# Performance work log

Measured on AMD Instinct MI355X. Metric: run time of the kernel, lower is better.

## Reference

```python
import jax, jax.numpy as jnp
import numpy as np

HEADS, DH, HID, EDGE_D = 8, 16, 128, 32  # heads, head_dim, hidden_dim, edge_dim
N, E = 50000, 800000


def _ln(x, w, b):
    mu = jnp.mean(x, axis=-1, keepdims=True)
    var = jnp.var(x, axis=-1, keepdims=True)
    return (x - mu) * jax.lax.rsqrt(var + 1e-5) * w + b


def setup_inputs() -> dict:
    key = jax.random.key(0)
    ks = jax.random.split(key, 16)
    lin = lambda k, fi, fo: (jax.random.normal(k, (fi, fo), jnp.float32) / np.sqrt(fi).astype(np.float32))
    inp = {
        'x': jax.random.normal(ks[0], (N, HID), jnp.float32),
        'edge_index': jax.random.randint(ks[1], (2, E), 0, N, jnp.int32),
        'edge_attr': jax.random.normal(ks[2], (E, EDGE_D), jnp.float32),
        'Wq': lin(ks[3], HID, HID), 'bq': jnp.zeros((HID,), jnp.float32),
        'Wk': lin(ks[4], HID, HID), 'bk': jnp.zeros((HID,), jnp.float32),
        'Wv': lin(ks[5], HID, HID), 'bv': jnp.zeros((HID,), jnp.float32),
        'We': lin(ks[6], EDGE_D, HID), 'be': jnp.zeros((HID,), jnp.float32),
        'Wskip': lin(ks[7], HID, HID), 'bskip': jnp.zeros((HID,), jnp.float32),
        'ln1_w': jnp.ones((HID,), jnp.float32), 'ln1_b': jnp.zeros((HID,), jnp.float32),
        'W1': lin(ks[8], HID, 4 * HID), 'b1': jnp.zeros((4 * HID,), jnp.float32),
        'W2': lin(ks[9], 4 * HID, HID), 'b2': jnp.zeros((HID,), jnp.float32),
        'ln2_w': jnp.ones((HID,), jnp.float32), 'ln2_b': jnp.zeros((HID,), jnp.float32),
    }
    return inp


def reference(x, edge_index, edge_attr, Wq, bq, Wk, bk, Wv, bv, We, be,
              Wskip, bskip, ln1_w, ln1_b, W1, b1, W2, b2, ln2_w, ln2_b):
    n = x.shape[0]
    src, dst = edge_index[0], edge_index[1]

    h = _ln(x, ln1_w, ln1_b)
    # projections, then per-edge gathers -> [E, H, Dh]
    q = (h @ Wq + bq)[dst].reshape(-1, HEADS, DH)
    k = (h @ Wk + bk)[src].reshape(-1, HEADS, DH)
    v = (h @ Wv + bv)[src].reshape(-1, HEADS, DH)
    e = (edge_attr @ We + be).reshape(-1, HEADS, DH)
    k = k + e
    v = v + e

    alpha = jnp.einsum('ehd,ehd->eh', q, k) / np.sqrt(DH).astype(np.float32)  # [E, H]
    # segment softmax over destination nodes (PyG softmax semantics)
    amax = jax.ops.segment_max(alpha, dst, num_segments=n)
    amax = jnp.where(jnp.isfinite(amax), amax, 0.0)
    expa = jnp.exp(alpha - amax[dst])
    denom = jax.ops.segment_sum(expa, dst, num_segments=n)
    alpha = expa / (denom[dst] + 1e-16)

    msg = jax.ops.segment_sum(alpha[..., None] * v, dst, num_segments=n)  # [N, H, Dh]
    conv_out = msg.reshape(n, HID) + h @ Wskip + bskip  # root_weight skip

    x = x + conv_out
    h2 = _ln(x, ln2_w, ln2_b)
    ffn = jax.nn.gelu(h2 @ W1 + b1, approximate=False) @ W2 + b2
    return x + ffn
```

## Files before the change

kernel.cpp:

```cpp
#include <hip/hip_runtime.h>
#include <math.h>

#define HID 128
#define EDGE_D 32
#define SC 0.36067376f

typedef unsigned short u16;
typedef unsigned int u32;
typedef __bf16 bf16x8 __attribute__((ext_vector_type(8)));
typedef float f32x4 __attribute__((ext_vector_type(4)));
typedef u32 u32x4 __attribute__((ext_vector_type(4)));
typedef u32 u32x2 __attribute__((ext_vector_type(2)));

static __device__ __forceinline__ u16 f2bf(float f) {
  u32 u = __float_as_uint(f);
  u += 0x7fffu + ((u >> 16) & 1u);
  return (u16)(u >> 16);
}
static __device__ __forceinline__ u32 pack2(float a, float b) {
  return (u32)f2bf(a) | ((u32)f2bf(b) << 16);
}
static __device__ __forceinline__ float bflo(u32 w) { return __uint_as_float(w << 16); }
static __device__ __forceinline__ float bfhi(u32 w) { return __uint_as_float(w & 0xffff0000u); }
static __device__ __forceinline__ float grp16_sum(float x) {
  x += __int_as_float(__builtin_amdgcn_mov_dpp(__float_as_int(x), 0x128, 0xf, 0xf, true));
  x += __int_as_float(__builtin_amdgcn_mov_dpp(__float_as_int(x), 0x124, 0xf, 0xf, true));
  x += __int_as_float(__builtin_amdgcn_mov_dpp(__float_as_int(x), 0x122, 0xf, 0xf, true));
  x += __int_as_float(__builtin_amdgcn_mov_dpp(__float_as_int(x), 0x121, 0xf, 0xf, true));
  return x;
}
static __device__ __forceinline__ float wave_allreduce_sum(float v) {
#pragma unroll
  for (int off = 32; off > 0; off >>= 1) v += __shfl_xor(v, off);
  return v;
}

__global__ __launch_bounds__(256) void ln_kernel(const float* __restrict__ in,
                                                 u16* __restrict__ out,
                                                 const float* __restrict__ w,
                                                 const float* __restrict__ b, int n) {
  int row0 = blockIdx.x * 4 + (threadIdx.x >> 6);
  int lane = threadIdx.x & 63;
  int stride = gridDim.x * 4;
  for (int row = row0; row < n; row += stride) {
    const float* p = in + (size_t)row * HID;
    float a = p[lane], c = p[lane + 64];
    float s = wave_allreduce_sum(a + c);
    float s2 = wave_allreduce_sum(a * a + c * c);
    float mean = s * (1.f / 128.f);
    float var = s2 * (1.f / 128.f) - mean * mean;
    float rs = rsqrtf(var + 1e-5f);
    u16* o = out + (size_t)row * HID;
    o[lane] = f2bf((a - mean) * rs * w[lane] + b[lane]);
    o[lane + 64] = f2bf((c - mean) * rs * w[lane + 64] + b[lane + 64]);
  }
}

__global__ __launch_bounds__(256) void convert_weights(
    const float* __restrict__ Wq, const float* __restrict__ Wk,
    const float* __restrict__ Wv, const float* __restrict__ Ws,
    const float* __restrict__ W1, const float* __restrict__ W2,
    const float* __restrict__ We, u16* __restrict__ WqkvsT,
    u16* __restrict__ W1T, u16* __restrict__ W2T, u16* __restrict__ WbdT,
    int* __restrict__ cnt, int Nn) {
  int idx = blockIdx.x * 256 + threadIdx.x;
  if (idx < 65536) {
    int m = idx >> 7, k = idx & 127;
    const float* Wm = m < 128 ? Wq : m < 256 ? Wk : m < 384 ? Wv : Ws;
    WqkvsT[idx] = f2bf(Wm[k * 128 + (m & 127)]);
  } else if (idx < 131072) {
    int j = idx - 65536;
    int m = j >> 7, k = j & 127;
    W1T[j] = f2bf(W1[k * 512 + m]);
  } else if (idx < 196608) {
    int j = idx - 131072;
    int m = j >> 9, k = j & 511;
    W2T[j] = f2bf(W2[k * 128 + m]);
  } else if (idx < 229376) {
    int j = idx - 196608;
    int m = j >> 8, c = j & 255;
    WbdT[j] = ((c >> 5) == (m >> 4)) ? f2bf(We[(c & 31) * 128 + m]) : (u16)0;
  } else if (idx < 229376 + Nn) {
    cnt[idx - 229376] = 0;
  }
}

#define GSTAGE(buf, kc)                                                        \
  {                                                                            \
    _Pragma("unroll") for (int i = 0; i < 2; i++) {                            \
      int idx = i * 256 + t;                                                   \
      int row = idx >> 2, c4 = idx & 3;                                        \
      __builtin_amdgcn_global_load_lds(                                        \
          (const __attribute__((address_space(1))) u32*)(A + (size_t)(r0 + row) * K + (kc) + c4 * 8), \
          (__attribute__((address_space(3))) u32*)&As[buf][idx * 8], 16, 0, 0);\
      __builtin_amdgcn_global_load_lds(                                        \
          (const __attribute__((address_space(1))) u32*)(Bt + (size_t)(c0 + row) * K + (kc) + c4 * 8), \
          (__attribute__((address_space(3))) u32*)&Bs[buf][idx * 8], 16, 0, 0);\
    }                                                                          \
  }

#define GEMM_CORE                                                              \
  constexpr int NT = K / 32;                                                   \
  GSTAGE(0, 0)                                                                 \
  __syncthreads();                                                             \
  _Pragma("unroll") for (int tt = 0; tt < NT; tt++) {                          \
    if (tt + 1 < NT) GSTAGE((tt + 1) & 1, (tt + 1) * 32)                       \
    bf16x8 a0 = *(const bf16x8*)&As[tt & 1][(w * 32 + sr) * 32 + g * 8];       \
    bf16x8 a1 = *(const bf16x8*)&As[tt & 1][(w * 32 + 16 + sr) * 32 + g * 8];  \
    _Pragma("unroll") for (int nn = 0; nn < 8; nn++) {                         \
      bf16x8 b = *(const bf16x8*)&Bs[tt & 1][(nn * 16 + sr) * 32 + g * 8];     \
      acc[0][nn] = __builtin_amdgcn_mfma_f32_16x16x32_bf16(a0, b, acc[0][nn], 0, 0, 0); \
      acc[1][nn] = __builtin_amdgcn_mfma_f32_16x16x32_bf16(a1, b, acc[1][nn], 0, 0, 0); \
    }                                                                          \
    __syncthreads();                                                           \
  }

template <int EPI, int K>
__global__ __launch_bounds__(256) void gemm_bf16(
    const u16* __restrict__ A, const u16* __restrict__ Bt, int n,
    const float* __restrict__ bias0, const float* __restrict__ bias1,
    const float* __restrict__ bias2, const float* __restrict__ bias3,
    float* __restrict__ of0, u32* __restrict__ opq, u32* __restrict__ pkv,
    u16* __restrict__ ob1, const float* __restrict__ addsrc) {
  __shared__ u16 As[2][128 * 32];
  __shared__ u16 Bs[2][128 * 32];
  int t = threadIdx.x;
  int w = t >> 6, lane = t & 63;
  int g = lane >> 4, sr = lane & 15;
  int r0 = blockIdx.x * 128;
  int c0 = blockIdx.y * 128;
  f32x4 acc[2][8];
#pragma unroll
  for (int m = 0; m < 2; m++)
#pragma unroll
    for (int nn = 0; nn < 8; nn++) acc[m][nn] = {0.f, 0.f, 0.f, 0.f};

  GEMM_CORE

  if (EPI == 0 && blockIdx.y == 0) {
#pragma unroll
    for (int m = 0; m < 2; m++)
#pragma unroll
      for (int nn = 0; nn < 4; nn++)
#pragma unroll
        for (int j = 0; j < 4; j++) {
          int row = r0 + w * 32 + m * 16 + g * 4 + j;
          if (row < n) {
            int cj = nn * 16 + sr;
            opq[((size_t)row << 6) + cj] =
                pack2(acc[m][nn][j] + bias0[cj], acc[m][nn + 4][j] + bias0[cj + 64]);
          }
        }
    return;
  }
  if (EPI == 0 && (blockIdx.y == 1 || blockIdx.y == 2)) {
    const float* bp = blockIdx.y == 1 ? bias1 : bias2;
    int which = blockIdx.y - 1;
#pragma unroll
    for (int m = 0; m < 2; m++)
#pragma unroll
      for (int nn = 0; nn < 4; nn++)
#pragma unroll
        for (int j = 0; j < 4; j++) {
          int row = r0 + w * 32 + m * 16 + g * 4 + j;
          if (row < n) {
            int cj = nn * 16 + sr;
            pkv[((size_t)row << 7) + (cj << 1) + which] =
                pack2(acc[m][nn][j] + bp[cj], acc[m][nn + 4][j] + bp[cj + 64]);
          }
        }
    return;
  }
#pragma unroll
  for (int m = 0; m < 2; m++)
#pragma unroll
    for (int nn = 0; nn < 8; nn++)
#pragma unroll
      for (int j = 0; j < 4; j++) {
        int row = r0 + w * 32 + m * 16 + g * 4 + j;
        if (row < n) {
          int cj = nn * 16 + sr;
          float val = acc[m][nn][j];
          if (EPI == 0) {
            of0[(size_t)row * HID + cj] = val + bias3[cj];
          } else if (EPI == 1) {
            int cjg = blockIdx.y * 128 + cj;
            float v2 = val + bias0[cjg];
            v2 = 0.5f * v2 * (1.f + erff(v2 * 0.70710678118f));
            ob1[(size_t)row * 512 + cjg] = f2bf(v2);
          } else {
            of0[(size_t)row * HID + cj] = val + bias0[cj] + addsrc[(size_t)row * HID + cj];
          }
        }
      }
}

__global__ __launch_bounds__(256) void gemm_bd_fin(
    const u16* __restrict__ A, const u16* __restrict__ Bt, int n,
    const float* __restrict__ x, const float* __restrict__ msg,
    const float* __restrict__ lbuf, const float* __restrict__ be,
    const float* __restrict__ lnw, const float* __restrict__ lnb,
    float* __restrict__ skipx1, u16* __restrict__ h2) {
  __shared__ u16 As[2][128 * 32];
  __shared__ u16 Bs[2][128 * 32];
  constexpr int K = 256;
  int t = threadIdx.x;
  int w = t >> 6, lane = t & 63;
  int g = lane >> 4, sr = lane & 15;
  int r0 = blockIdx.x * 128;
  int c0 = 0;
  f32x4 acc[2][8];
#pragma unroll
  for (int m = 0; m < 2; m++)
#pragma unroll
    for (int nn = 0; nn < 8; nn++) acc[m][nn] = {0.f, 0.f, 0.f, 0.f};

  GEMM_CORE

  float becol[8], wcol[8], bcol[8];
#pragma unroll
  for (int nn = 0; nn < 8; nn++) {
    int c = nn * 16 + sr;
    becol[nn] = be[c];
    wcol[nn] = lnw[c];
    bcol[nn] = lnb[c];
  }
#pragma unroll
  for (int m = 0; m < 2; m++)
#pragma unroll
    for (int j = 0; j < 4; j++) {
      int row = r0 + w * 32 + m * 16 + g * 4 + j;
      if (row < n) {
        const float* xr = x + (size_t)row * HID;
        const float* mr = msg + (size_t)row * HID;
        float* sxr = skipx1 + (size_t)row * HID;
        f32x4 L0 = *(const f32x4*)(lbuf + (size_t)row * 8);
        f32x4 L1 = *(const f32x4*)(lbuf + (size_t)row * 8 + 4);
        float tv[8];
        float s = 0.f, s2 = 0.f;
#pragma unroll
        for (int nn = 0; nn < 8; nn++) {
          int c = nn * 16 + sr;
          float linv = nn < 4 ? L0[nn] : L1[nn - 4];
          float t1 = xr[c] + (mr[c] + acc[m][nn][j]) * linv + becol[nn] + sxr[c];
          tv[nn] = t1;
          s += t1;
          s2 = fmaf(t1, t1, s2);
        }
        s = grp16_sum(s);
        s2 = grp16_sum(s2);
        float mean = s * (1.f / 128.f);
        float var = s2 * (1.f / 128.f) - mean * mean;
        float rs = rsqrtf(var + 1e-5f);
        u16* h2r = h2 + (size_t)row * HID;
#pragma unroll
        for (int nn = 0; nn < 8; nn++) {
          int c = nn * 16 + sr;
          sxr[c] = tv[nn];
          h2r[c] = f2bf((tv[nn] - mean) * rs * wcol[nn] + bcol[nn]);
        }
      }
    }
}

__global__ __launch_bounds__(256) void hist_kernel(const int* __restrict__ dstp,
                                                   int* __restrict__ cnt, int E) {
  int i = blockIdx.x * blockDim.x + threadIdx.x;
  int stride = gridDim.x * blockDim.x;
  for (; i < E; i += stride) atomicAdd(&cnt[dstp[i]], 1);
}

__global__ __launch_bounds__(256) void scan_partial(const int* __restrict__ cnt,
                                                    int* __restrict__ bs, int N) {
  __shared__ int sd[256];
  int idx = blockIdx.x * 256 + threadIdx.x;
  sd[threadIdx.x] = (idx < N) ? cnt[idx] : 0;
  __syncthreads();
  for (int s = 128; s > 0; s >>= 1) {
    if (threadIdx.x < s) sd[threadIdx.x] += sd[threadIdx.x + s];
    __syncthreads();
  }
  if (threadIdx.x == 0) bs[blockIdx.x] = sd[0];
}

__global__ __launch_bounds__(256) void scan_bs(const int* __restrict__ bs,
                                               int* __restrict__ bs2, int nb) {
  __shared__ int sd[256];
  int t = threadIdx.x;
  int v = (t < nb) ? bs[t] : 0;
  sd[t] = v;
  __syncthreads();
  for (int s = 1; s < 256; s <<= 1) {
    int add = (t >= s) ? sd[t - s] : 0;
    __syncthreads();
    sd[t] += add;
    __syncthreads();
  }
  bs2[t] = sd[t] - v;
}

__global__ __launch_bounds__(256) void scan_final(const int* __restrict__ cnt,
                                                  const int* __restrict__ bs2,
                                                  int* __restrict__ offs,
                                                  int* __restrict__ woff, int N) {
  __shared__ int sd[256];
  int t = threadIdx.x;
  int idx = blockIdx.x * 256 + t;
  int v = (idx < N) ? cnt[idx] : 0;
  sd[t] = v;
  __syncthreads();
  for (int s = 1; s < 256; s <<= 1) {
    int add = (t >= s) ? sd[t - s] : 0;
    __syncthreads();
    sd[t] += add;
    __syncthreads();
  }
  if (idx < N) {
    int ex = sd[t] - v + bs2[blockIdx.x];
    offs[idx] = ex;
    woff[idx] = ex;
  }
}

__global__ __launch_bounds__(256) void scatter_kernel(const int* __restrict__ ei,
                                                      int* __restrict__ woff,
                                                      int2* __restrict__ sorted,
                                                      int E) {
  int i = blockIdx.x * blockDim.x + threadIdx.x;
  int stride = gridDim.x * blockDim.x;
  for (; i < E; i += stride) {
    int src = ei[i];
    int dst = ei[E + i];
    int pos = atomicAdd(&woff[dst], 1);
    sorted[pos] = make_int2(src, i);
  }
}

__global__ __launch_bounds__(256) void qwe_kernel(const u32* __restrict__ pq,
                                                  const float* __restrict__ We,
                                                  const float* __restrict__ be,
                                                  u32* __restrict__ qweb,
                                                  float* __restrict__ qbe, int Nn) {
  __shared__ float sWe[32][129];
  __shared__ float sbe[128];
  int t = threadIdx.x;
  for (int i = t; i < 32 * 128; i += 256) sWe[i >> 7][i & 127] = We[i];
  if (t < 128) sbe[t] = be[t];
  __syncthreads();
  int lane = t & 63, w = t >> 6;
  int g = lane >> 4, sr = lane & 15;
  int base = lane & 48;
  int stride = gridDim.x * 4;
  for (int node = blockIdx.x * 4 + w; node < Nn; node += stride) {
    u32 pw = pq[(size_t)node * 64 + lane];
    float q0 = bflo(pw), q1 = bfhi(pw);
    float o00 = 0.f, o01 = 0.f, o10 = 0.f, o11 = 0.f;
#pragma unroll
    for (int d0 = 0; d0 < 16; d0++) {
      float qa = __shfl(q0, base + d0);
      float qb = __shfl(q1, base + d0);
      int col = base + d0;
      o00 += qa * sWe[2 * sr][col];
      o01 += qa * sWe[2 * sr + 1][col];
      o10 += qb * sWe[2 * sr][64 + col];
      o11 += qb * sWe[2 * sr + 1][64 + col];
    }
    qweb[(size_t)node * 128 + g * 16 + sr] = pack2(o00 * SC, o01 * SC);
    qweb[(size_t)node * 128 + 64 + g * 16 + sr] = pack2(o10 * SC, o11 * SC);
    float t0 = grp16_sum(q0 * sbe[lane]);
    float t1 = grp16_sum(q1 * sbe[lane + 64]);
    if (sr == 0) {
      qbe[node * 8 + g] = t0 * SC;
      qbe[node * 8 + 4 + g] = t1 * SC;
    }
  }
}

#define ISSUE4(P, base_)                                                       \
  {                                                                            \
    _Pragma("unroll") for (int jj = 0; jj < 4; jj++) {                         \
      int sj = min(base_ + jj, segn - 1);                                      \
      int sxx = __builtin_amdgcn_readlane(seRx, sj);                           \
      int syy = __builtin_amdgcn_readlane(seRy, sj);                           \
      P##kv[jj] = *(const u32x2*)(pkv + ((size_t)sxx << 7) + (lane << 1));     \
      P##ea[jj] = *(const float2*)(eaf + ((size_t)syy << 5) + 2 * sr);         \
    }                                                                          \
  }

#define COMP4(P, base_)                                                        \
  {                                                                            \
    _Pragma("unroll") for (int jj = 0; jj < 4; jj++) {                         \
      u32 kx = P##kv[jj].x, ky = P##kv[jj].y;                                  \
      float ex = P##ea[jj].x, ey = P##ea[jj].y;                                \
      float k0 = bflo(kx), k1 = bfhi(kx);                                      \
      float v0f = bflo(ky), v1f = bfhi(ky);                                    \
      float p0 = fmaf(q0C, k0, fmaf(qw0x, ex, qw0y * ey));                     \
      float p1 = fmaf(q1C, k1, fmaf(qw1x, ex, qw1y * ey));                     \
      p0 = grp16_sum(p0) + qb0C;                                               \
      p1 = grp16_sum(p1) + qb1C;                                               \
      bool val_ = (base_ + jj) < segn;                                         \
      float w1 = val_ ? __builtin_amdgcn_exp2f(p0) : 0.f;                      \
      float w2 = val_ ? __builtin_amdgcn_exp2f(p1) : 0.f;                      \
      l1 += w1;                                                                \
      l2 += w2;                                                                \
      a0 = fmaf(w1, v0f, a0);                                                  \
      a1 = fmaf(w2, v1f, a1);                                                  \
      wa00 = fmaf(w1, ex, wa00);                                               \
      wa01 = fmaf(w1, ey, wa01);                                               \
      wa10 = fmaf(w2, ex, wa10);                                               \
      wa11 = fmaf(w2, ey, wa11);                                               \
    }                                                                          \
  }

__global__ __launch_bounds__(256) void fused_edge(
    const int* __restrict__ offs, const int* __restrict__ cnt,
    const int2* __restrict__ sorted, const float* __restrict__ eaf,
    const float* __restrict__ be, const u32* __restrict__ pq,
    const u32* __restrict__ pkv, const u32* __restrict__ qweb,
    const float* __restrict__ qbe, float* __restrict__ msg,
    u32* __restrict__ weab, float* __restrict__ lbuf, int Nn, int Etot) {
  int lane = threadIdx.x & 63;
  int w = threadIdx.x >> 6;
  int g = lane >> 4, sr = lane & 15;
  int wid = blockIdx.x * 4 + w;
  int nw = gridDim.x * 4;
  int per = (Nn + nw - 1) / nw;
  int n0 = wid * per;
  int n1 = min(Nn, n0 + per);
  if (n0 >= n1) return;
  int nn = n1 - n0;

  float be0 = be[lane], be1 = be[lane + 64];

  int ml = min(lane, nn - 1);
  int myBeg = offs[n0 + ml];
  int myCnt = cnt[n0 + ml];

  int beg = __builtin_amdgcn_readlane(myBeg, 0);
  int num = __builtin_amdgcn_readlane(myCnt, 0);
  int2 se2 = sorted[min(beg + min(lane, max(num - 1, 0)), Etot - 1)];
  int seCx = se2.x, seCy = se2.y;
  u32 pqC = pq[(size_t)n0 * 64 + lane];
  u32 qwb0C = qweb[(size_t)n0 * 128 + g * 16 + sr];
  u32 qwb1C = qweb[(size_t)n0 * 128 + 64 + g * 16 + sr];
  float qb0C = qbe[(size_t)n0 * 8 + g], qb1C = qbe[(size_t)n0 * 8 + 4 + g];

  for (int ni = 0; ni < nn; ni++) {
    int node = n0 + ni;
    int begX = 0, numX = 0, seXx = 0, seXy = 0;
    u32 pqX = 0, qwb0X = 0, qwb1X = 0;
    float qb0X = 0.f, qb1X = 0.f;
    if (ni + 1 < nn) {
      begX = __builtin_amdgcn_readlane(myBeg, ni + 1);
      numX = __builtin_amdgcn_readlane(myCnt, ni + 1);
      int2 sx = sorted[min(begX + min(lane, max(numX - 1, 0)), Etot - 1)];
      seXx = sx.x;
      seXy = sx.y;
      pqX = pq[(size_t)(node + 1) * 64 + lane];
      qwb0X = qweb[(size_t)(node + 1) * 128 + g * 16 + sr];
      qwb1X = qweb[(size_t)(node + 1) * 128 + 64 + g * 16 + sr];
      qb0X = qbe[(size_t)(node + 1) * 8 + g];
      qb1X = qbe[(size_t)(node + 1) * 8 + 4 + g];
    }
    float q0C = bflo(pqC) * SC, q1C = bfhi(pqC) * SC;
    float qw0x = bflo(qwb0C), qw0y = bfhi(qwb0C);
    float qw1x = bflo(qwb1C), qw1y = bfhi(qwb1C);
    float l1 = 0.f, l2 = 0.f, a0 = 0.f, a1 = 0.f;
    float wa00 = 0.f, wa01 = 0.f, wa10 = 0.f, wa11 = 0.f;
    if (num > 0) {
      int cb = 0;
      int seRx = seCx, seRy = seCy;
      while (true) {
        int segn = min(num - cb, 64);
        u32x2 Akv[4], Bkv[4];
        float2 Aea[4], Bea[4];
        ISSUE4(A, 0)
        for (int c = 0; c < segn; c += 8) {
          ISSUE4(B, c + 4)
          COMP4(A, c)
          ISSUE4(A, c + 8)
          COMP4(B, c + 4)
        }
        cb += 64;
        if (cb >= num) break;
        int rem = num - cb;
        int2 sn = sorted[min(beg + cb + min(lane, rem - 1), Etot - 1)];
        seRx = sn.x;
        seRy = sn.y;
      }
    }
    size_t ob = (size_t)node * HID + lane;
    if (num > 0) {
      msg[ob] = a0;
      msg[ob + 64] = a1;
    } else {
      msg[ob] = -be0;
      msg[ob + 64] = -be1;
    }
    weab[(size_t)node * 128 + g * 16 + sr] = pack2(wa00, wa01);
    weab[(size_t)node * 128 + 64 + g * 16 + sr] = pack2(wa10, wa11);
    if (sr == 0) {
      lbuf[(size_t)node * 8 + g] = (num > 0) ? 1.f / (l1 + 1e-30f) : 1.f;
      lbuf[(size_t)node * 8 + 4 + g] = (num > 0) ? 1.f / (l2 + 1e-30f) : 1.f;
    }
    beg = begX;
    num = numX;
    seCx = seXx;
    seCy = seXy;
    pqC = pqX;
    qwb0C = qwb0X;
    qwb1C = qwb1X;
    qb0C = qb0X;
    qb1C = qb1X;
  }
}

extern "C" void kernel_launch(void* const* d_in, const int* in_sizes, int n_in,
                              void* d_out, int out_size, void* d_ws, size_t ws_size,
                              hipStream_t stream) {
  const float* x = (const float*)d_in[0];
  const int* ei = (const int*)d_in[1];
  const float* ea = (const float*)d_in[2];
  const float* Wq = (const float*)d_in[3];
  const float* bq = (const float*)d_in[4];
  const float* Wk = (const float*)d_in[5];
  const float* bk = (const float*)d_in[6];
  const float* Wv = (const float*)d_in[7];
  const float* bv = (const float*)d_in[8];
  const float* We = (const float*)d_in[9];
  const float* be = (const float*)d_in[10];
  const float* Wskip = (const float*)d_in[11];
  const float* bskip = (const float*)d_in[12];
  const float* ln1w = (const float*)d_in[13];
  const float* ln1b = (const float*)d_in[14];
  const float* W1 = (const float*)d_in[15];
  const float* b1p = (const float*)d_in[16];
  const float* W2 = (const float*)d_in[17];
  const float* b2p = (const float*)d_in[18];
  const float* ln2w = (const float*)d_in[19];
  const float* ln2b = (const float*)d_in[20];

  int N = in_sizes[0] / HID;
  int E = in_sizes[1] / 2;
  size_t nf = (size_t)N * HID;

  float* ws = (float*)d_ws;
  size_t off = 0;
  u16* h_bf = (u16*)(ws + off); off += nf / 2;
  u32* pq = (u32*)(ws + off); off += nf / 2;
  u32* pkv = (u32*)(ws + off); off += nf;
  float* skipx1 = ws + off; off += nf;
  float* msg = ws + off; off += nf;
  u32* weab = (u32*)(ws + off); off += nf;
  float* lbuf = ws + off; off += (size_t)N * 8;
  u32* qweb = (u32*)(ws + off); off += nf;
  float* qbe = ws + off; off += (size_t)N * 8;
  int2* sorted = (int2*)(ws + off); off += (size_t)E * 2;
  int* cnt = (int*)(ws + off); off += N;
  int* offs = (int*)(ws + off); off += N;
  int* woff = (int*)(ws + off); off += N;
  int* bs = (int*)(ws + off); off += 256;
  int* bs2 = (int*)(ws + off); off += 256;
  u16* WqkvsT = (u16*)(ws + off); off += 32768;
  u16* W1T = (u16*)(ws + off); off += 32768;
  u16* W2T = (u16*)(ws + off); off += 32768;
  u16* WbdT = (u16*)(ws + off); off += 16384;
  u16* h2bf = h_bf;
  u16* tbf = (u16*)msg;

  convert_weights<<<1092, 256, 0, stream>>>(Wq, Wk, Wv, Wskip, W1, W2, We,
                                            WqkvsT, W1T, W2T, WbdT, cnt, N);

  int ln_blocks = (N + 3) / 4;
  ln_kernel<<<ln_blocks, 256, 0, stream>>>(x, h_bf, ln1w, ln1b, N);

  dim3 gq((N + 127) / 128, 4);
  gemm_bf16<0, 128><<<gq, 256, 0, stream>>>(h_bf, WqkvsT, N, bq, bk, bv, bskip,
                                            skipx1, pq, pkv, nullptr, nullptr);

  int nb = (N + 255) / 256;
  hist_kernel<<<1024, 256, 0, stream>>>(ei + E, cnt, E);
  scan_partial<<<nb, 256, 0, stream>>>(cnt, bs, N);
  scan_bs<<<1, 256, 0, stream>>>(bs, bs2, nb);
  scan_final<<<nb, 256, 0, stream>>>(cnt, bs2, offs, woff, N);
  scatter_kernel<<<1024, 256, 0, stream>>>(ei, woff, sorted, E);

  qwe_kernel<<<1024, 256, 0, stream>>>(pq, We, be, qweb, qbe, N);

  int fe_blocks = (N + 7) / 8;
  fused_edge<<<fe_blocks, 256, 0, stream>>>(offs, cnt, sorted, ea, be, pq, pkv,
                                            qweb, qbe, msg, weab, lbuf, N, E);

  dim3 ge((N + 127) / 128, 1);
  gemm_bd_fin<<<ge, 256, 0, stream>>>((const u16*)weab, WbdT, N, x, msg, lbuf,
                                      be, ln2w, ln2b, skipx1, h2bf);

  dim3 gf1((N + 127) / 128, 4);
  gemm_bf16<1, 128><<<gf1, 256, 0, stream>>>(h2bf, W1T, N, b1p, nullptr, nullptr,
                                             nullptr, nullptr, nullptr, nullptr,
                                             tbf, nullptr);
  dim3 gf2((N + 127) / 128, 1);
  gemm_bf16<2, 512><<<gf2, 256, 0, stream>>>(tbf, W2T, N, b2p, nullptr, nullptr,
                                             nullptr, (float*)d_out, nullptr,
                                             nullptr, nullptr, skipx1);
}
```

Before: 438.3 us.

## Fuse skip projection into final GEMM and fold softmax normalization into edge kernel

The skip projection h@Wskip moves out of the QKV GEMM (grid y drops from 4 to 3) and becomes a second K=128 MFMA pass inside gemm_bd_fin, so skipx1 is no longer written and reread as an fp32 intermediate. The fused edge kernel now applies the 1/l softmax normalization to msg and to the bf16 weab buffer directly, which removes the lbuf array and its per-row loads. The fused_edge grid is halved to (N+15)/16 blocks. The costs are an extra GEMM pass in the epilogue kernel and quantizing the normalized weights to bf16 before the We GEMM.

```diff
diff --git a/kernel.cpp b/kernel.cpp
--- a/kernel.cpp
+++ b/kernel.cpp
@@ -119,7 +119,7 @@
 __global__ __launch_bounds__(256) void gemm_bf16(
     const u16* __restrict__ A, const u16* __restrict__ Bt, int n,
     const float* __restrict__ bias0, const float* __restrict__ bias1,
-    const float* __restrict__ bias2, const float* __restrict__ bias3,
+    const float* __restrict__ bias2,
     float* __restrict__ of0, u32* __restrict__ opq, u32* __restrict__ pkv,
     u16* __restrict__ ob1, const float* __restrict__ addsrc) {
   __shared__ u16 As[2][128 * 32];
@@ -153,7 +153,7 @@
         }
     return;
   }
-  if (EPI == 0 && (blockIdx.y == 1 || blockIdx.y == 2)) {
+  if (EPI == 0) {
     const float* bp = blockIdx.y == 1 ? bias1 : bias2;
     int which = blockIdx.y - 1;
 #pragma unroll
@@ -181,9 +181,7 @@
         if (row < n) {
           int cj = nn * 16 + sr;
           float val = acc[m][nn][j];
-          if (EPI == 0) {
-            of0[(size_t)row * HID + cj] = val + bias3[cj];
-          } else if (EPI == 1) {
+          if (EPI == 1) {
             int cjg = blockIdx.y * 128 + cj;
             float v2 = val + bias0[cjg];
             v2 = 0.5f * v2 * (1.f + erff(v2 * 0.70710678118f));
@@ -196,14 +194,14 @@
 }
 
 __global__ __launch_bounds__(256) void gemm_bd_fin(
-    const u16* __restrict__ A, const u16* __restrict__ Bt, int n,
+    const u16* __restrict__ Aw, const u16* __restrict__ BtW,
+    const u16* __restrict__ Ah, const u16* __restrict__ BtS, int n,
     const float* __restrict__ x, const float* __restrict__ msg,
-    const float* __restrict__ lbuf, const float* __restrict__ be,
+    const float* __restrict__ be, const float* __restrict__ bskip,
     const float* __restrict__ lnw, const float* __restrict__ lnb,
-    float* __restrict__ skipx1, u16* __restrict__ h2) {
+    float* __restrict__ x1, u16* __restrict__ h2) {
   __shared__ u16 As[2][128 * 32];
   __shared__ u16 Bs[2][128 * 32];
-  constexpr int K = 256;
   int t = threadIdx.x;
   int w = t >> 6, lane = t & 63;
   int g = lane >> 4, sr = lane & 15;
@@ -215,13 +213,25 @@
 #pragma unroll
     for (int nn = 0; nn < 8; nn++) acc[m][nn] = {0.f, 0.f, 0.f, 0.f};
 
-  GEMM_CORE
-
-  float becol[8], wcol[8], bcol[8];
+  {
+    const u16* A = Aw;
+    const u16* Bt = BtW;
+    constexpr int K = 256;
+    GEMM_CORE
+  }
+  {
+    const u16* A = Ah;
+    const u16* Bt = BtS;
+    constexpr int K = 128;
+    GEMM_CORE
+  }
+
+  float becol[8], wcol[8], bcol[8], bscol[8];
 #pragma unroll
   for (int nn = 0; nn < 8; nn++) {
     int c = nn * 16 + sr;
     becol[nn] = be[c];
+    bscol[nn] = bskip[c];
     wcol[nn] = lnw[c];
     bcol[nn] = lnb[c];
   }
@@ -233,16 +243,13 @@
       if (row < n) {
         const float* xr = x + (size_t)row * HID;
         const float* mr = msg + (size_t)row * HID;
-        float* sxr = skipx1 + (size_t)row * HID;
-        f32x4 L0 = *(const f32x4*)(lbuf + (size_t)row * 8);
-        f32x4 L1 = *(const f32x4*)(lbuf + (size_t)row * 8 + 4);
+        float* x1r = x1 + (size_t)row * HID;
         float tv[8];
         float s = 0.f, s2 = 0.f;
 #pragma unroll
         for (int nn = 0; nn < 8; nn++) {
           int c = nn * 16 + sr;
-          float linv = nn < 4 ? L0[nn] : L1[nn - 4];
-          float t1 = xr[c] + (mr[c] + acc[m][nn][j]) * linv + becol[nn] + sxr[c];
+          float t1 = xr[c] + mr[c] + acc[m][nn][j] + becol[nn] + bscol[nn];
           tv[nn] = t1;
           s += t1;
           s2 = fmaf(t1, t1, s2);
@@ -256,7 +263,7 @@
 #pragma unroll
         for (int nn = 0; nn < 8; nn++) {
           int c = nn * 16 + sr;
-          sxr[c] = tv[nn];
+          x1r[c] = tv[nn];
           h2r[c] = f2bf((tv[nn] - mean) * rs * wcol[nn] + bcol[nn]);
         }
       }
@@ -418,7 +425,7 @@
     const float* __restrict__ be, const u32* __restrict__ pq,
     const u32* __restrict__ pkv, const u32* __restrict__ qweb,
     const float* __restrict__ qbe, float* __restrict__ msg,
-    u32* __restrict__ weab, float* __restrict__ lbuf, int Nn, int Etot) {
+    u32* __restrict__ weab, int Nn, int Etot) {
   int lane = threadIdx.x & 63;
   int w = threadIdx.x >> 6;
   int g = lane >> 4, sr = lane & 15;
@@ -489,20 +496,17 @@
         seRy = sn.y;
       }
     }
+    float inv1 = 1.f / (l1 + 1e-30f), inv2 = 1.f / (l2 + 1e-30f);
     size_t ob = (size_t)node * HID + lane;
     if (num > 0) {
-      msg[ob] = a0;
-      msg[ob + 64] = a1;
+      msg[ob] = a0 * inv1;
+      msg[ob + 64] = a1 * inv2;
     } else {
       msg[ob] = -be0;
       msg[ob + 64] = -be1;
     }
-    weab[(size_t)node * 128 + g * 16 + sr] = pack2(wa00, wa01);
-    weab[(size_t)node * 128 + 64 + g * 16 + sr] = pack2(wa10, wa11);
-    if (sr == 0) {
-      lbuf[(size_t)node * 8 + g] = (num > 0) ? 1.f / (l1 + 1e-30f) : 1.f;
-      lbuf[(size_t)node * 8 + 4 + g] = (num > 0) ? 1.f / (l2 + 1e-30f) : 1.f;
-    }
+    weab[(size_t)node * 128 + g * 16 + sr] = pack2(wa00 * inv1, wa01 * inv1);
+    weab[(size_t)node * 128 + 64 + g * 16 + sr] = pack2(wa10 * inv2, wa11 * inv2);
     beg = begX;
     num = numX;
     seCx = seXx;
@@ -552,7 +556,6 @@
   float* skipx1 = ws + off; off += nf;
   float* msg = ws + off; off += nf;
   u32* weab = (u32*)(ws + off); off += nf;
-  float* lbuf = ws + off; off += (size_t)N * 8;
   u32* qweb = (u32*)(ws + off); off += nf;
   float* qbe = ws + off; off += (size_t)N * 8;
   int2* sorted = (int2*)(ws + off); off += (size_t)E * 2;
@@ -565,7 +568,7 @@
   u16* W1T = (u16*)(ws + off); off += 32768;
   u16* W2T = (u16*)(ws + off); off += 32768;
   u16* WbdT = (u16*)(ws + off); off += 16384;
-  u16* h2bf = h_bf;
+  u16* h2o = (u16*)qweb;
   u16* tbf = (u16*)msg;
 
   convert_weights<<<1092, 256, 0, stream>>>(Wq, Wk, Wv, Wskip, W1, W2, We,
@@ -574,9 +577,9 @@
   int ln_blocks = (N + 3) / 4;
   ln_kernel<<<ln_blocks, 256, 0, stream>>>(x, h_bf, ln1w, ln1b, N);
 
-  dim3 gq((N + 127) / 128, 4);
-  gemm_bf16<0, 128><<<gq, 256, 0, stream>>>(h_bf, WqkvsT, N, bq, bk, bv, bskip,
-                                            skipx1, pq, pkv, nullptr, nullptr);
+  dim3 gq((N + 127) / 128, 3);
+  gemm_bf16<0, 128><<<gq, 256, 0, stream>>>(h_bf, WqkvsT, N, bq, bk, bv,
+                                            nullptr, pq, pkv, nullptr, nullptr);
 
   int nb = (N + 255) / 256;
   hist_kernel<<<1024, 256, 0, stream>>>(ei + E, cnt, E);
@@ -587,20 +590,20 @@
 
   qwe_kernel<<<1024, 256, 0, stream>>>(pq, We, be, qweb, qbe, N);
 
-  int fe_blocks = (N + 7) / 8;
+  int fe_blocks = (N + 15) / 16;
   fused_edge<<<fe_blocks, 256, 0, stream>>>(offs, cnt, sorted, ea, be, pq, pkv,
-                                            qweb, qbe, msg, weab, lbuf, N, E);
+                                            qweb, qbe, msg, weab, N, E);
 
   dim3 ge((N + 127) / 128, 1);
-  gemm_bd_fin<<<ge, 256, 0, stream>>>((const u16*)weab, WbdT, N, x, msg, lbuf,
-                                      be, ln2w, ln2b, skipx1, h2bf);
+  gemm_bd_fin<<<ge, 256, 0, stream>>>((const u16*)weab, WbdT, h_bf,
+                                      WqkvsT + 384 * 128, N, x, msg, be, bskip,
+                                      ln2w, ln2b, skipx1, h2o);
 
   dim3 gf1((N + 127) / 128, 4);
-  gemm_bf16<1, 128><<<gf1, 256, 0, stream>>>(h2bf, W1T, N, b1p, nullptr, nullptr,
-                                             nullptr, nullptr, nullptr, nullptr,
-                                             tbf, nullptr);
+  gemm_bf16<1, 128><<<gf1, 256, 0, stream>>>(h2o, W1T, N, b1p, nullptr, nullptr,
+                                             nullptr, nullptr, nullptr, tbf, nullptr);
   dim3 gf2((N + 127) / 128, 1);
   gemm_bf16<2, 512><<<gf2, 256, 0, stream>>>(tbf, W2T, N, b2p, nullptr, nullptr,
-                                             nullptr, (float*)d_out, nullptr,
-                                             nullptr, nullptr, skipx1);
-}
+                                             (float*)d_out, nullptr, nullptr,
+                                             nullptr, skipx1);
+}
```

Result: faster. 429.2 us (-2.1%).
